# Optimization experiments

Measured on AMD Instinct MI355X. Metric: run time of the kernel, lower is better.

Reference implementation:

```python
import jax, jax.numpy as jnp
import numpy as np
from jax import lax

# 8 neighbor offsets of the Moore neighborhood (matches neighbors_roll_axes)
OFFS = [(i, j) for i in range(-1, 2) for j in range(-1, 2) if not (i == 0 and j == 0)]


def _neighbors(g):
    # g: [B,1,H,W]; toroidal shifts
    return [jnp.roll(g, (i, j), axis=(2, 3)) for i, j in OFFS]


def _binary_step(gb):
    # Conway rule on boolean grid: alive if sum==3 or (alive and sum==2)
    s = sum(n.astype(jnp.int32) for n in _neighbors(gb))
    return (s == 3) | (gb & (s == 2))


def _prob_step(p):
    # P(next alive) = P(exactly 3 of 8 neighbors alive) + P(exactly 2 alive) * p
    # Computed via a count-distribution DP over the 8 independent Bernoulli
    # neighbors -- mathematically identical to the C(8,2)+C(8,3)=84 enumerated
    # products in the torch code, but O(8) fused elementwise passes.
    z = jnp.zeros_like(p)
    c0, c1, c2, c3 = jnp.ones_like(p), z, z, z  # P(count==k); >=4 absorbed
    for q in _neighbors(p):
        c3 = c3 * (1 - q) + c2 * q
        c2 = c2 * (1 - q) + c1 * q
        c1 = c1 * (1 - q) + c0 * q
        c0 = c0 * (1 - q)
    return c3 + c2 * p


def _cconv(x, w, b, pad):
    # circular ('wrap') padding conv, NCHW/OIHW
    if pad:
        x = jnp.pad(x, ((0, 0), (0, 0), (pad, pad), (pad, pad)), mode='wrap')
    y = lax.conv_general_dilated(x, w, (1, 1), 'VALID',
                                 dimension_numbers=('NCHW', 'OIHW', 'NCHW'))
    return y + b[None, :, None, None]


def _block(x, xp, params):
    w1, b1, w2, b2, w3, b3, w4, b4 = params
    # stencil features computed under no_grad in the original
    xp_bin = lax.stop_gradient(xp > 0.5)
    x_pred_bin = _binary_step(xp_bin)
    x_pred = lax.stop_gradient(_prob_step(lax.stop_gradient(xp)))
    h = jnp.concatenate([x, xp, xp_bin.astype(x.dtype), x_pred,
                         x_pred_bin.astype(x.dtype)], axis=1)  # [B,5,H,W]
    h = jax.nn.relu(_cconv(h, w1, b1, 2))
    h = jax.nn.relu(_cconv(h, w2, b2, 1))
    h = jax.nn.relu(_cconv(h, w3, b3, 0))
    return jax.nn.sigmoid(_cconv(h, w4, b4, 1))


def setup_inputs() -> dict:
    key = jax.random.key(0)
    ks = jax.random.split(key, 6)
    B, H, W = 4, 256, 256
    x = jax.random.uniform(ks[0], (B, 1, H, W), jnp.float32)

    def wi(k, shape):
        fan_in = shape[1] * shape[2] * shape[3]
        return (jax.random.normal(k, shape, jnp.float32) / np.sqrt(fan_in)).astype(jnp.float32)

    w1 = wi(ks[1], (256, 5, 5, 5));   b1 = jnp.zeros((256,), jnp.float32)
    w2 = wi(ks[2], (256, 256, 3, 3)); b2 = jnp.zeros((256,), jnp.float32)
    w3 = wi(ks[3], (256, 256, 1, 1)); b3 = jnp.zeros((256,), jnp.float32)
    w4 = wi(ks[4], (1, 256, 3, 3));   b4 = jnp.zeros((1,), jnp.float32)
    return {"x": x, "w1": w1, "b1": b1, "w2": w2, "b2": b2,
            "w3": w3, "b3": b3, "w4": w4, "b4": b4, "n_it": 5}


def reference(x, w1, b1, w2, b2, w3, b3, w4, b4, n_it):
    params = (w1, b1, w2, b2, w3, b3, w4, b4)
    xp = x
    for _ in range(n_it):
        xp = _block(x, xp, params)
    return xp
```

## Files before the change

### kernel.cpp

```cpp
#include <hip/hip_runtime.h>
#include <hip/hip_bf16.h>


#define NPIX (4 * 256 * 256)

typedef double v4d __attribute__((ext_vector_type(4)));

__global__ __launch_bounds__(64) void probe_mode(int* __restrict__ modep)
{
    int lr = threadIdx.x & 15;
    v4d p1 = {}, p2 = {};
    p1 = __builtin_amdgcn_mfma_f64_16x16x4f64((double)lr, 1.0, p1, 0, 0, 0);
    p2 = __builtin_amdgcn_mfma_f64_16x16x4f64(1.0, (double)lr, p2, 0, 0, 0);
    double v1 = __shfl(p1[0], 16);
    double v2 = __shfl(p2[0], 16);
    if (threadIdx.x == 0)
        *modep = (v1 == 16.0) ? 0 : (v1 == 4.0) ? 1 : (v2 == 16.0) ? 2 : 3;
}

__global__ __launch_bounds__(256) void xinit_kernel(
    const float* __restrict__ x, double* __restrict__ xp64)
{
    int p = blockIdx.x * 256 + threadIdx.x;
    xp64[p] = (double)x[p];
}

__global__ __launch_bounds__(256) void stencil_strip(
    const float* __restrict__ x, const double* __restrict__ xp,
    double* __restrict__ h0, size_t h0_is,
    int job0, int ns_shift, int R)
{
    int slot = blockIdx.y;
    int j = job0 + slot;
    int img = j >> ns_shift;
    int r0 = (j & ((1 << ns_shift) - 1)) * R;
    int pbase = img << 16;
    int y = (r0 - 4 + blockIdx.x) & 255;
    int col = threadIdx.x;
    double q[8];
    int s = 0, idx = 0;
    #pragma unroll
    for (int i = -1; i <= 1; ++i)
        #pragma unroll
        for (int jj = -1; jj <= 1; ++jj) {
            if (i == 0 && jj == 0) continue;
            int ys = (y - i) & 255, xs = (col - jj) & 255;
            double v = xp[pbase + ((ys << 8) | xs)];
            q[idx++] = v;
            s += (v > 0.5) ? 1 : 0;
        }
    double c = xp[pbase + ((y << 8) | col)];
    bool alive = c > 0.5;
    bool binnext = (s == 3) || (alive && s == 2);
    double c0 = 1.0, c1 = 0.0, c2 = 0.0, c3 = 0.0;
    #pragma unroll
    for (int k = 0; k < 8; ++k) {
        double qq = q[k], r = 1.0 - qq;
        c3 = c3 * r + c2 * qq;
        c2 = c2 * r + c1 * qq;
        c1 = c1 * r + c0 * qq;
        c0 = c0 * r;
    }
    double xpred = c3 + c2 * c;
    double* o = h0 + slot * h0_is + ((size_t)blockIdx.x * 256 + col) * 8;
    o[0] = (double)x[pbase + ((y << 8) | col)];
    o[1] = c;
    o[2] = alive ? 1.0 : 0.0;
    o[3] = xpred;
    o[4] = binnext ? 1.0 : 0.0;
    o[5] = 0.0; o[6] = 0.0; o[7] = 0.0;
}

template<int CIN, int TK, int KH, int KW>
__global__ __launch_bounds__(512, 2) void conv_gemm(
    const double* __restrict__ A,
    size_t a_is,
    const double* __restrict__ Wp,
    const float* __restrict__ bias,
    double* __restrict__ O,
    size_t o_is,
    int delta,
    const int* __restrict__ modep)
{
    constexpr int PW = KW / 2, PH = KH / 2;
    constexpr int CHUNKS = CIN / TK;
    constexpr int NCH = KH * KW * CHUNKS;
    __shared__ double Asmem[2][TK][66];
    __shared__ double Wsmem[2][TK][130];

    const double* Ai = A + blockIdx.z * a_is;
    double* Oi = O + blockIdx.z * o_is;
    const int mode = *modep;

    const int tid = threadIdx.x;
    const int pm0 = blockIdx.x * 64;
    const int on0 = blockIdx.y * 128;
    const int wave = tid >> 6, lane = tid & 63;
    const bool prod = wave >= 4;

    const int ptid = tid & 255;
    constexpr int LPP = TK / 2;
    constexpr int PPR = 256 / LPP;
    constexpr int ROUNDS = 64 / PPR;
    const int part = ptid % LPP;
    const int pixA = ptid / LPP;
    const int wrow = ptid >> 6;
    const int wcol = (ptid & 63) << 1;

    const int lq = lane >> 4, lr = lane & 15;
    const int wr = ((wave & 3) >> 1) * 32;
    const int wc = (wave & 1) * 64;

    v4d acc[2][4] = {};

    auto stage = [&](int ch, int buf) {
        int tap = ch / CHUNKS, cc = ch % CHUNKS;
        int dy = tap / KW - PH, dx = tap % KW - PW;
        int c0 = cc * TK;
        int kglob = tap * CIN + c0;
        #pragma unroll
        for (int r = 0; r < TK / 4; ++r) {
            int row = r * 4 + wrow;
            *(double2*)&Wsmem[buf][row][wcol] =
                *(const double2*)&Wp[(size_t)(kglob + row) * 256 + on0 + wcol];
        }
        #pragma unroll
        for (int r = 0; r < ROUNDS; ++r) {
            int pix = r * PPR + pixA;
            int pl = pm0 + pix;
            int yl = pl >> 8, col = pl & 255;
            int xs = (col + dx) & 255;
            int srcpx = ((yl + dy + delta) << 8) | xs;
            double2 v = *(const double2*)(Ai + (size_t)srcpx * CIN + c0 + part * 2);
            Asmem[buf][part * 2 + 0][pix] = v.x;
            Asmem[buf][part * 2 + 1][pix] = v.y;
        }
    };

    if (prod) stage(0, 0);
    __syncthreads();
    for (int ch = 0; ch < NCH; ++ch) {
        const int cur = ch & 1;
        if (prod) {
            if (ch + 1 < NCH) stage(ch + 1, cur ^ 1);
        } else {
            #pragma unroll
            for (int k0 = 0; k0 < TK / 4; ++k0) {
                const int kk = k0 * 4 + lq;
                double a[2], b[4];
                a[0] = Asmem[cur][kk][wr + lr];
                a[1] = Asmem[cur][kk][wr + 16 + lr];
                #pragma unroll
                for (int ct = 0; ct < 4; ++ct)
                    b[ct] = Wsmem[cur][kk][wc + ct * 16 + lr];
                #pragma unroll
                for (int rt = 0; rt < 2; ++rt)
                    #pragma unroll
                    for (int ct = 0; ct < 4; ++ct)
                        acc[rt][ct] = __builtin_amdgcn_mfma_f64_16x16x4f64(
                            a[rt], b[ct], acc[rt][ct], 0, 0, 0);
            }
        }
        __syncthreads();
    }

    if (!prod) {
        #pragma unroll
        for (int rt = 0; rt < 2; ++rt)
            #pragma unroll
            for (int ct = 0; ct < 4; ++ct)
                #pragma unroll
                for (int i = 0; i < 4; ++i) {
                    int hq = lq * 4 + i, hi = i * 4 + lq;
                    int rl = (mode == 0) ? hq : (mode == 1) ? hi : lr;
                    int cl = (mode <= 1) ? lr : (mode == 2) ? hq : hi;
                    int px = pm0 + wr + rt * 16 + rl;
                    int oc = on0 + wc + ct * 16 + cl;
                    Oi[(size_t)px * 256 + oc] =
                        fmax(acc[rt][ct][i] + (double)bias[oc], 0.0);
                }
    }
}

__global__ __launch_bounds__(256) void conv4_sig(
    const double* __restrict__ H3, size_t h3_is,
    const float* __restrict__ w4, const float* __restrict__ b4,
    float* __restrict__ out, double* __restrict__ xp_new,
    int job0, int ns_shift, int R)
{
    __shared__ double w4s[2304];
    int tid = threadIdx.x;
    for (int i = tid; i < 2304; i += 256) w4s[i] = (double)w4[i];
    __syncthreads();
    int slot = blockIdx.y;
    int j = job0 + slot;
    int img = j >> ns_shift;
    int r0 = (j & ((1 << ns_shift) - 1)) * R;
    const double* H3i = H3 + slot * h3_is;
    int pbase = img << 16;
    int lane = tid & 63, wv = tid >> 6;
    int p0 = blockIdx.x * 64 + wv * 16;
    for (int pi = 0; pi < 16; ++pi) {
        int pl = p0 + pi;
        int yl = pl >> 8, col = pl & 255;
        double acc = 0.0;
        #pragma unroll
        for (int tap = 0; tap < 9; ++tap) {
            int row = yl + tap / 3 - 1 + 1;
            int xs = (col + tap % 3 - 1) & 255;
            const double* src = H3i + (size_t)((row << 8) | xs) * 256;
            #pragma unroll
            for (int jj = 0; jj < 4; ++jj) {
                int c = lane + 64 * jj;
                acc = fma(src[c], w4s[c * 9 + tap], acc);
            }
        }
        #pragma unroll
        for (int off = 32; off; off >>= 1) acc += __shfl_xor(acc, off, 64);
        if (lane == 0) {
            double v = acc + (double)b4[0];
            double s = 1.0 / (1.0 + exp(-v));
            int p = pbase + (((r0 + yl) << 8) | col);
            out[p] = (float)s;
            xp_new[p] = s;
        }
    }
}

__global__ void repack_w1(const float* __restrict__ w1, double* __restrict__ W1p) {
    int t = blockIdx.x * 256 + threadIdx.x;
    if (t >= 25 * 8 * 256) return;
    int oc = t & 255, cin = (t >> 8) & 7, tap = t >> 11;
    W1p[t] = (cin < 5) ? (double)w1[oc * 125 + cin * 25 + tap] : 0.0;
}
__global__ void repack_w2(const float* __restrict__ w2, double* __restrict__ W2p) {
    int t = blockIdx.x * 256 + threadIdx.x;
    if (t >= 9 * 256 * 256) return;
    int oc = t & 255, cin = (t >> 8) & 255, tap = t >> 16;
    W2p[t] = (double)w2[((oc << 8) | cin) * 9 + tap];
}
__global__ void repack_w3(const float* __restrict__ w3, double* __restrict__ W3p) {
    int t = blockIdx.x * 256 + threadIdx.x;
    if (t >= 256 * 256) return;
    int oc = t & 255, cin = t >> 8;
    W3p[t] = (double)w3[oc * 256 + cin];
}

extern "C" void kernel_launch(void* const* d_in, const int* in_sizes, int n_in,
                              void* d_out, int out_size, void* d_ws, size_t ws_size,
                              hipStream_t stream)
{
    const float* x  = (const float*)d_in[0];
    const float* w1 = (const float*)d_in[1];
    const float* b1 = (const float*)d_in[2];
    const float* w2 = (const float*)d_in[3];
    const float* b2 = (const float*)d_in[4];
    const float* w3 = (const float*)d_in[5];
    const float* b3 = (const float*)d_in[6];
    const float* w4 = (const float*)d_in[7];
    const float* b4 = (const float*)d_in[8];
    float* out = (float*)d_out;

    char* ws = (char*)d_ws;
    double* W1p = (double*)(ws);
    double* W2p = (double*)(ws + 409600ull);
    double* W3p = (double*)(ws + 5128192ull);
    double* xpA = (double*)(ws + 5652480ull);
    double* xpB = (double*)(ws + 7749632ull);
    int*   modep = (int*)(ws + 9846784ull);
    char*  bufs = ws + 9847040ull;
    const size_t base_need = 9847040ull;
    const size_t ROWD  = 524288ull;
    const size_t ROWH0 = 16384ull;

    const int cand_r[14] = {64, 128, 256, 64, 32, 64, 16, 32, 16, 8, 8, 4, 4, 2};
    const int cand_g[14] = { 4,   2,   1,  3,  4,  2,  4,  2,  2, 4, 2, 2, 1, 1};
    int R = 2, G = 1;
    for (int ci = 0; ci < 14; ++ci) {
        int r = cand_r[ci], g = cand_g[ci];
        size_t need = base_need + (size_t)g *
            ((size_t)(r + 8) * ROWH0 + (size_t)(2 * r + 6) * ROWD);
        if (ws_size >= need) { R = r; G = g; break; }
    }
    int ns_shift = 0;
    while ((256 >> ns_shift) != R) ++ns_shift;
    const int NSTRIP = 256 / R;
    const int jobs = 4 * NSTRIP;

    double* h0 = (double*)bufs;
    double* h1 = (double*)(bufs + (size_t)G * (R + 8) * ROWH0);
    double* h2 = (double*)((char*)h1 + (size_t)G * (R + 4) * ROWD);
    double* h3 = h1;
    const size_t h0_is = (size_t)(R + 8) * 256 * 8;
    const size_t h1_is = (size_t)(R + 4) * 256 * 256;
    const size_t h2_is = (size_t)(R + 2) * 256 * 256;

    probe_mode<<<1, 64, 0, stream>>>(modep);
    repack_w1<<<200, 256, 0, stream>>>(w1, W1p);
    repack_w2<<<2304, 256, 0, stream>>>(w2, W2p);
    repack_w3<<<256, 256, 0, stream>>>(w3, W3p);
    xinit_kernel<<<NPIX / 256, 256, 0, stream>>>(x, xpA);

    for (int it = 0; it < 5; ++it) {
        const double* xp_rd = (it & 1) ? xpB : xpA;
        double*       xp_wr = (it & 1) ? xpA : xpB;
        for (int j0 = 0; j0 < jobs; j0 += G) {
            int g = (jobs - j0 < G) ? (jobs - j0) : G;
            stencil_strip<<<dim3(R + 8, g), 256, 0, stream>>>(
                x, xp_rd, h0, h0_is, j0, ns_shift, R);
            conv_gemm<8, 8, 5, 5><<<dim3((R + 4) * 4, 2, g), 512, 0, stream>>>(
                h0, h0_is, W1p, b1, h1, h1_is, 2, modep);
            conv_gemm<256, 16, 3, 3><<<dim3((R + 2) * 4, 2, g), 512, 0, stream>>>(
                h1, h1_is, W2p, b2, h2, h2_is, 1, modep);
            conv_gemm<256, 16, 1, 1><<<dim3((R + 2) * 4, 2, g), 512, 0, stream>>>(
                h2, h2_is, W3p, b3, h3, h1_is, 0, modep);
            conv4_sig<<<dim3(R * 4, g), 256, 0, stream>>>(
                h3, h1_is, w4, b4, out, xp_wr, j0, ns_shift, R);
        }
    }
}
```

Before: 43.75 ms.

## Add specialized 3x3 conv kernel reusing staged input rows across horizontal taps

Replaces the generic conv_gemm for the 256->256 3x3 layer with a dedicated kernel that stages one input row segment (66 pixels, 8 channels) per chunk and reuses it for all three horizontal taps. It loads weights for all three dx taps together, so the number of chunks drops and A-tile global loads are shared across taps instead of being re-fetched per tap. It also raises the scheduling priority of the MFMA consumer waves with s_setprio in both GEMM kernels. The trade-off is a larger weight shared-memory buffer and smaller K per chunk (8 channels), which could affect occupancy or the balance between producer and consumer waves.

Result: faster. 41.49 ms (-5.2%).

```diff
diff --git a/kernel.cpp b/kernel.cpp
--- a/kernel.cpp
+++ b/kernel.cpp
@@ -73,14 +73,11 @@
 
 template<int CIN, int TK, int KH, int KW>
 __global__ __launch_bounds__(512, 2) void conv_gemm(
-    const double* __restrict__ A,
-    size_t a_is,
+    const double* __restrict__ A, size_t a_is,
     const double* __restrict__ Wp,
     const float* __restrict__ bias,
-    double* __restrict__ O,
-    size_t o_is,
-    int delta,
-    const int* __restrict__ modep)
+    double* __restrict__ O, size_t o_is,
+    int delta, const int* __restrict__ modep)
 {
     constexpr int PW = KW / 2, PH = KH / 2;
     constexpr int CHUNKS = CIN / TK;
@@ -97,6 +94,7 @@
     const int on0 = blockIdx.y * 128;
     const int wave = tid >> 6, lane = tid & 63;
     const bool prod = wave >= 4;
+    if (!prod) asm volatile("s_setprio 1");
 
     const int ptid = tid & 255;
     constexpr int LPP = TK / 2;
@@ -182,6 +180,118 @@
     }
 }
 
+__global__ __launch_bounds__(512, 2) void conv2_gemm(
+    const double* __restrict__ A, size_t a_is,
+    const double* __restrict__ Wp,
+    const float* __restrict__ bias,
+    double* __restrict__ O, size_t o_is,
+    const int* __restrict__ modep)
+{
+    __shared__ double Asmem[2][8][66];
+    __shared__ double Wsmem[2][24][130];
+
+    const double* Ai = A + blockIdx.z * a_is;
+    double* Oi = O + blockIdx.z * o_is;
+    const int mode = *modep;
+
+    const int tid = threadIdx.x;
+    const int pm0 = blockIdx.x * 64;
+    const int on0 = blockIdx.y * 128;
+    const int yrow = pm0 >> 8;
+    const int col0 = pm0 & 255;
+    const int wave = tid >> 6, lane = tid & 63;
+    const bool prod = wave >= 4;
+    if (!prod) asm volatile("s_setprio 1");
+
+    const int ptid = tid & 255;
+    const int lq = lane >> 4, lr = lane & 15;
+    const int wr = ((wave & 3) >> 1) * 32;
+    const int wc = (wave & 1) * 64;
+
+    v4d acc[2][4] = {};
+
+    auto stage = [&](int ch, int buf) {
+        int dy = ch >> 5;
+        int cc = ch & 31;
+        int c0 = cc * 8;
+        int srow = yrow + dy;
+        {
+            int px = ptid >> 2, pp = ptid & 3;
+            int xs = (col0 - 1 + px) & 255;
+            double2 v = *(const double2*)(
+                Ai + (size_t)((srow << 8) | xs) * 256 + c0 + pp * 2);
+            Asmem[buf][pp * 2 + 0][px] = v.x;
+            Asmem[buf][pp * 2 + 1][px] = v.y;
+            if (ptid < 8) {
+                int t2 = 256 + ptid;
+                int px2 = t2 >> 2, pp2 = t2 & 3;
+                int xs2 = (col0 - 1 + px2) & 255;
+                double2 v2 = *(const double2*)(
+                    Ai + (size_t)((srow << 8) | xs2) * 256 + c0 + pp2 * 2);
+                Asmem[buf][pp2 * 2 + 0][px2] = v2.x;
+                Asmem[buf][pp2 * 2 + 1][px2] = v2.y;
+            }
+        }
+        #pragma unroll
+        for (int i = 0; i < 6; ++i) {
+            int t = ptid + 256 * i;
+            int row = t >> 6;
+            int cp = (t & 63) << 1;
+            int tap = dy * 3 + (row >> 3);
+            int k = tap * 256 + c0 + (row & 7);
+            *(double2*)&Wsmem[buf][row][cp] =
+                *(const double2*)&Wp[(size_t)k * 256 + on0 + cp];
+        }
+    };
+
+    if (prod) stage(0, 0);
+    __syncthreads();
+    for (int ch = 0; ch < 96; ++ch) {
+        const int cur = ch & 1;
+        if (prod) {
+            if (ch + 1 < 96) stage(ch + 1, cur ^ 1);
+        } else {
+            #pragma unroll
+            for (int dx = 0; dx < 3; ++dx)
+                #pragma unroll
+                for (int k0 = 0; k0 < 2; ++k0) {
+                    const int kA = k0 * 4 + lq;
+                    const int kW = dx * 8 + k0 * 4 + lq;
+                    double a[2], b[4];
+                    a[0] = Asmem[cur][kA][dx + wr + lr];
+                    a[1] = Asmem[cur][kA][dx + wr + 16 + lr];
+                    #pragma unroll
+                    for (int ct = 0; ct < 4; ++ct)
+                        b[ct] = Wsmem[cur][kW][wc + ct * 16 + lr];
+                    #pragma unroll
+                    for (int rt = 0; rt < 2; ++rt)
+                        #pragma unroll
+                        for (int ct = 0; ct < 4; ++ct)
+                            acc[rt][ct] = __builtin_amdgcn_mfma_f64_16x16x4f64(
+                                a[rt], b[ct], acc[rt][ct], 0, 0, 0);
+                }
+        }
+        __syncthreads();
+    }
+
+    if (!prod) {
+        #pragma unroll
+        for (int rt = 0; rt < 2; ++rt)
+            #pragma unroll
+            for (int ct = 0; ct < 4; ++ct)
+                #pragma unroll
+                for (int i = 0; i < 4; ++i) {
+                    int hq = lq * 4 + i, hi = i * 4 + lq;
+                    int rl = (mode == 0) ? hq : (mode == 1) ? hi : lr;
+                    int cl = (mode <= 1) ? lr : (mode == 2) ? hq : hi;
+                    int px = pm0 + wr + rt * 16 + rl;
+                    int oc = on0 + wc + ct * 16 + cl;
+                    Oi[(size_t)px * 256 + oc] =
+                        fmax(acc[rt][ct][i] + (double)bias[oc], 0.0);
+                }
+    }
+}
+
 __global__ __launch_bounds__(256) void conv4_sig(
     const double* __restrict__ H3, size_t h3_is,
     const float* __restrict__ w4, const float* __restrict__ b4,
@@ -310,8 +420,8 @@
                 x, xp_rd, h0, h0_is, j0, ns_shift, R);
             conv_gemm<8, 8, 5, 5><<<dim3((R + 4) * 4, 2, g), 512, 0, stream>>>(
                 h0, h0_is, W1p, b1, h1, h1_is, 2, modep);
-            conv_gemm<256, 16, 3, 3><<<dim3((R + 2) * 4, 2, g), 512, 0, stream>>>(
-                h1, h1_is, W2p, b2, h2, h2_is, 1, modep);
+            conv2_gemm<<<dim3((R + 2) * 4, 2, g), 512, 0, stream>>>(
+                h1, h1_is, W2p, b2, h2, h2_is, modep);
             conv_gemm<256, 16, 1, 1><<<dim3((R + 2) * 4, 2, g), 512, 0, stream>>>(
                 h2, h2_is, W3p, b3, h3, h1_is, 0, modep);
             conv4_sig<<<dim3(R * 4, g), 256, 0, stream>>>(
```
